# Optimization experiments

Measured on AMD Instinct MI355X. Metric: run time of the kernel, lower is better.

The kernel has to match this reference:

```python
import jax, jax.numpy as jnp
import numpy as np

EPS = 1e-6
NUM_HEADS = 8


def setup_inputs() -> dict:
    key0 = jax.random.key(0)
    ks = jax.random.split(key0, 8)
    N, B, C, HW = 900, 8, 256, 1156

    def lin(k):
        kw, kb = jax.random.split(k)
        W = jax.random.normal(kw, (C, C), jnp.float32) * 0.02
        b = jax.random.normal(kb, (C,), jnp.float32) * 0.02
        return W, b

    Wq, bq = lin(ks[0])
    Wk, bk = lin(ks[1])
    Wv, bv = lin(ks[2])
    Wo, bo = lin(ks[3])
    query = jax.random.normal(ks[4], (N, B, C), jnp.float32)
    key = jax.random.normal(ks[5], (HW, B, C), jnp.float32)
    query_pos = jax.random.normal(ks[6], (N, B, C), jnp.float32)
    key_pos = jax.random.normal(ks[7], (HW, B, C), jnp.float32)
    return dict(query=query, key=key, query_pos=query_pos, key_pos=key_pos,
                Wq=Wq, bq=bq, Wk=Wk, bk=bk, Wv=Wv, bv=bv, Wo=Wo, bo=bo)


def reference(query, key, query_pos, key_pos, Wq, bq, Wk, bk, Wv, bv, Wo, bo):
    # Faithful port of LinearCrossAttention.forward (value=None -> key,
    # identity=None -> query, batch_first=False, dropout inactive).
    # NOTE: the original permutes to (B, seq, head, head_dim) but then applies
    # cumsum(dim=2) / einsums along axis 2, i.e. over the HEAD axis; we
    # reproduce that exactly.
    N, B, C = query.shape
    HW = key.shape[0]
    H = NUM_HEADS
    D = C // H

    q = (query @ Wq.T + bq) + query_pos          # (N,B,C)
    k = (key @ Wk.T + bk) + key_pos              # (HW,B,C)
    v = key @ Wv.T + bv                          # (HW,B,C)

    q = jnp.transpose(q.reshape(N, B, H, D), (1, 0, 2, 3))    # (B,N,H,D)
    k = jnp.transpose(k.reshape(HW, B, H, D), (1, 0, 2, 3))   # (B,HW,H,D)
    v = jnp.transpose(v.reshape(HW, B, H, D), (1, 0, 2, 3))   # (B,HW,H,D)

    q = jax.nn.sigmoid(q)
    k = jax.nn.sigmoid(k)

    if HW > N:  # pad queries along the sequence axis
        q = jnp.concatenate([q, jnp.zeros((B, HW - N, H, D), q.dtype)], axis=1)

    dot = lambda a, b: jnp.sum(a * b, axis=-1)   # 'nhld,nhld->nhl'

    sink_incoming = 1.0 / dot(q + EPS, jnp.cumsum(k, axis=2) + EPS)   # (B,HW,H)
    source_outgoing = 1.0 / dot(k + EPS, jnp.cumsum(q, axis=2) + EPS)
    normal = (jnp.arange(H, dtype=q.dtype) + 1.0)[None, None, :]       # (1,1,H)
    sink_incoming = sink_incoming * normal
    source_outgoing = source_outgoing * normal

    conserved_sink = dot(q + EPS, jnp.cumsum(k * source_outgoing[..., None], axis=2) + EPS) / normal
    conserved_source = dot(k + EPS, jnp.cumsum(q * sink_incoming[..., None], axis=2) + EPS) / normal
    conserved_source = jnp.clip(conserved_source, -1.0, 1.0)

    sink_allocation = jax.nn.sigmoid(conserved_sink)
    conserved_source = jnp.exp(conserved_source)
    source_competition = conserved_source / jnp.cumsum(conserved_source, axis=-1) * normal

    # causal_dot_product with cumsum over axis 2 (head axis in this layout)
    qs = q * (sink_incoming[..., None] / normal[..., None])            # (B,HW,H,D)
    kv = jnp.cumsum(jnp.einsum('blhd,blhm->blhdm', k, v * source_competition[..., None]), axis=2)
    qkv = jnp.einsum('blhd,blhdm->blhm', qs, kv)                       # (B,HW,H,D)

    out = (qkv * sink_allocation[..., None])[:, :N]                    # (B,N,H,D)
    out = jnp.swapaxes(out, 1, 2).reshape(B, N, C)                     # matches torch transpose(1,2).reshape
    out = out @ Wo.T + bo
    out = jnp.swapaxes(out, 0, 1)                                      # (N,B,C)
    return query + out
```

## Files before the change

### kernel.cpp

```cpp
#include <hip/hip_runtime.h>
#include <math.h>

#define EPSV 1e-6f
constexpr int N_ = 900, B_ = 8, C_ = 256, H_ = 8, D_ = 32;
constexpr int M_TOT = N_ * B_;
constexpr int BM  = 32;
constexpr int NBLK = M_TOT / BM;
constexpr int BM2 = 32;
constexpr int VS  = 272;
constexpr int OFF_AQ = 65536;
constexpr int OFF_AK = 81920;
constexpr int OFF_Q  = 98304;
constexpr int OFF_K  = OFF_Q + BM * VS * 2;
constexpr int OFF_V  = OFF_K + BM * VS * 2;
constexpr int LDS1   = OFF_V + BM * VS * 2;
constexpr int LDS2   = 81920;

typedef __attribute__((ext_vector_type(8))) short short8;
typedef __attribute__((ext_vector_type(4))) float f32x4;
typedef __attribute__((ext_vector_type(4))) unsigned short us4;

__device__ __forceinline__ unsigned short f2bf(float f) {
    unsigned int u = __float_as_uint(f);
    return (unsigned short)((u + 0x7FFFu + ((u >> 16) & 1u)) >> 16);
}
__device__ __forceinline__ float bf2f(unsigned short u) {
    return __uint_as_float(((unsigned int)u) << 16);
}
__device__ __forceinline__ int swz(int row, int kElem) {
    int b = (row << 9) + (kElem << 1);
    return b ^ ((row & 7) << 4);
}
__device__ __forceinline__ float red8(float v) {
    v += __shfl_xor(v, 1); v += __shfl_xor(v, 2); v += __shfl_xor(v, 4);
    return v;
}

__global__ __launch_bounds__(256)
void pack_w(const float* __restrict__ Wq, const float* __restrict__ Wk,
            const float* __restrict__ Wv, const float* __restrict__ Wo,
            unsigned short* __restrict__ wbf)
{
    const int i = (blockIdx.x * 256 + threadIdx.x) * 8;
    const float* src = (i < 65536) ? Wq : (i < 131072) ? Wk
                     : (i < 196608) ? Wv : Wo;
    const int off = i & 65535;
    const float4 a = *reinterpret_cast<const float4*>(src + off);
    const float4 b = *reinterpret_cast<const float4*>(src + off + 4);
    short8 p;
    p[0]=(short)f2bf(a.x); p[1]=(short)f2bf(a.y);
    p[2]=(short)f2bf(a.z); p[3]=(short)f2bf(a.w);
    p[4]=(short)f2bf(b.x); p[5]=(short)f2bf(b.y);
    p[6]=(short)f2bf(b.z); p[7]=(short)f2bf(b.w);
    *reinterpret_cast<short8*>(wbf + i) = p;
}

__device__ __forceinline__ void stageW(const unsigned short* Wmat, int kkElem,
                                       char* wbufLds, int cw, int lane)
{
    #pragma unroll
    for (int n = 0; n < 8; ++n) {
        const int L  = n * 1024 + lane * 16;
        const int cl = L >> 7;
        const int kb = (L & 127) ^ ((cl & 7) << 4);
        const char* src = (const char*)Wmat + (size_t)(cw + cl) * 512
                        + kkElem * 2 + kb;
        __builtin_amdgcn_global_load_lds(
            (const __attribute__((address_space(1))) unsigned int*)src,
            (__attribute__((address_space(3))) unsigned int*)(wbufLds + n * 1024),
            16, 0, 0);
    }
}

__device__ __forceinline__ void step_mm(const unsigned char* At, const char* wb,
                                        int kkA, int lrow, int kg8,
                                        f32x4 acc[2][4])
{
    #pragma unroll
    for (int kh = 0; kh < 2; ++kh) {
        const short8 a0 = *reinterpret_cast<const short8*>(At + swz(lrow,      kkA + kh*32 + kg8));
        const short8 a1 = *reinterpret_cast<const short8*>(At + swz(16 + lrow, kkA + kh*32 + kg8));
        #pragma unroll
        for (int j = 0; j < 4; ++j) {
            const int cl = j*16 + lrow;
            const short8 bfr = *reinterpret_cast<const short8*>(
                wb + cl*128 + ((kh*64 + kg8*2) ^ ((cl & 7) << 4)));
            acc[0][j] = __builtin_amdgcn_mfma_f32_16x16x32_bf16(a0, bfr, acc[0][j], 0, 0, 0);
            acc[1][j] = __builtin_amdgcn_mfma_f32_16x16x32_bf16(a1, bfr, acc[1][j], 0, 0, 0);
        }
    }
}

__global__ __launch_bounds__(256)
void fused_qkva(const float* __restrict__ query, const float* __restrict__ key,
                const float* __restrict__ qpos,  const float* __restrict__ kpos,
                const unsigned short* __restrict__ wbf,
                const float* __restrict__ bq, const float* __restrict__ bk,
                const float* __restrict__ bv,
                unsigned short* __restrict__ abf)
{
    extern __shared__ char smem[];
    char* Wb = smem;
    unsigned char* Aq = (unsigned char*)(smem + OFF_AQ);
    unsigned char* Ak = (unsigned char*)(smem + OFF_AK);
    unsigned short* q_sb = (unsigned short*)(smem + OFF_Q);
    unsigned short* k_sb = (unsigned short*)(smem + OFF_K);
    unsigned short* v_sb = (unsigned short*)(smem + OFF_V);

    const int tid = threadIdx.x;
    const int r0  = blockIdx.x * BM;
    const int wave = tid >> 6, lane = tid & 63;
    const int cw = wave * 64;
    char* mywb = Wb + wave * 16384;

    stageW(wbf, 0, mywb, cw, lane);

    {
        const int trow = tid >> 5, k0 = (tid & 31) * 8;
        #pragma unroll
        for (int i = 0; i < 4; ++i) {
            const int row = trow + i * 8;
            const float* xr = query + (size_t)(r0 + row) * C_ + k0;
            const float4 a0 = *reinterpret_cast<const float4*>(xr);
            const float4 a1 = *reinterpret_cast<const float4*>(xr + 4);
            short8 pa;
            pa[0]=(short)f2bf(a0.x); pa[1]=(short)f2bf(a0.y);
            pa[2]=(short)f2bf(a0.z); pa[3]=(short)f2bf(a0.w);
            pa[4]=(short)f2bf(a1.x); pa[5]=(short)f2bf(a1.y);
            pa[6]=(short)f2bf(a1.z); pa[7]=(short)f2bf(a1.w);
            *reinterpret_cast<short8*>(Aq + swz(row, k0)) = pa;
            const float* kr = key + (size_t)(r0 + row) * C_ + k0;
            const float4 b0 = *reinterpret_cast<const float4*>(kr);
            const float4 b1 = *reinterpret_cast<const float4*>(kr + 4);
            short8 pb;
            pb[0]=(short)f2bf(b0.x); pb[1]=(short)f2bf(b0.y);
            pb[2]=(short)f2bf(b0.z); pb[3]=(short)f2bf(b0.w);
            pb[4]=(short)f2bf(b1.x); pb[5]=(short)f2bf(b1.y);
            pb[6]=(short)f2bf(b1.z); pb[7]=(short)f2bf(b1.w);
            *reinterpret_cast<short8*>(Ak + swz(row, k0)) = pb;
        }
    }

    const int lrow = lane & 15, kg8 = (lane >> 4) * 8;
    const int crow0 = (lane >> 4) * 4, ccol = lane & 15;

    float qp[32], kp[32], bqv[4], bkv[4], bvv[4];
    #pragma unroll
    for (int j = 0; j < 4; ++j) {
        const int ch = cw + j*16 + ccol;
        bqv[j] = bq[ch]; bkv[j] = bk[ch]; bvv[j] = bv[ch];
        #pragma unroll
        for (int rh = 0; rh < 2; ++rh)
            #pragma unroll
            for (int r_ = 0; r_ < 4; ++r_) {
                const int gr = r0 + rh*16 + crow0 + r_;
                qp[j*8+rh*4+r_] = qpos[(size_t)gr * C_ + ch];
                kp[j*8+rh*4+r_] = kpos[(size_t)gr * C_ + ch];
            }
    }

    __syncthreads();

    f32x4 qacc[2][4] = {}; f32x4 kacc[2][4] = {}; f32x4 vacc[2][4] = {};

    #pragma unroll
    for (int s = 0; s < 12; ++s) {
        if (s < 11) {
            const int nx = s + 1;
            stageW(wbf + (nx >> 2) * 65536, (nx & 3) * 64,
                   mywb + (nx & 1) * 8192, cw, lane);
            asm volatile("s_waitcnt vmcnt(8)" ::: "memory");
        } else {
            asm volatile("s_waitcnt vmcnt(0)" ::: "memory");
        }

        const char* wb = mywb + (s & 1) * 8192;
        const int kkA = (s & 3) * 64;
        if (s < 4)      step_mm(Aq, wb, kkA, lrow, kg8, qacc);
        else if (s < 8) step_mm(Ak, wb, kkA, lrow, kg8, kacc);
        else            step_mm(Ak, wb, kkA, lrow, kg8, vacc);

        if (s == 3) {
            #pragma unroll
            for (int j = 0; j < 4; ++j) {
                const int ch = cw + j*16 + ccol;
                #pragma unroll
                for (int rh = 0; rh < 2; ++rh)
                    #pragma unroll
                    for (int r_ = 0; r_ < 4; ++r_) {
                        float v = qacc[rh][j][r_] + bqv[j] + qp[j*8+rh*4+r_];
                        q_sb[(rh*16+crow0+r_)*VS + ch] = f2bf(1.f/(1.f+expf(-v)));
                    }
            }
        }
        if (s == 7) {
            #pragma unroll
            for (int j = 0; j < 4; ++j) {
                const int ch = cw + j*16 + ccol;
                #pragma unroll
                for (int rh = 0; rh < 2; ++rh)
                    #pragma unroll
                    for (int r_ = 0; r_ < 4; ++r_) {
                        float v = kacc[rh][j][r_] + bkv[j] + kp[j*8+rh*4+r_];
                        k_sb[(rh*16+crow0+r_)*VS + ch] = f2bf(1.f/(1.f+expf(-v)));
                    }
            }
        }
        if (s == 11) {
            #pragma unroll
            for (int j = 0; j < 4; ++j) {
                const int ch = cw + j*16 + ccol;
                #pragma unroll
                for (int rh = 0; rh < 2; ++rh)
                    #pragma unroll
                    for (int r_ = 0; r_ < 4; ++r_)
                        v_sb[(rh*16+crow0+r_)*VS + ch] =
                            f2bf(vacc[rh][j][r_] + bvv[j]);
            }
        }
    }

    __syncthreads();

    {
        const int loc = tid >> 3, tt = tid & 7, d0 = tt * 4;
        const int gr = r0 + loc;
        const int nn = gr >> 3, bb = gr & 7;
        const unsigned short* qr = q_sb + loc * VS + d0;
        const unsigned short* kr = k_sb + loc * VS + d0;
        const unsigned short* vr = v_sb + loc * VS + d0;
        f32x4 qh[8], kh[8], vh[8];
        #pragma unroll
        for (int h = 0; h < 8; ++h) {
            const us4 tq = *reinterpret_cast<const us4*>(qr + (h << 5));
            const us4 tk = *reinterpret_cast<const us4*>(kr + (h << 5));
            const us4 tv = *reinterpret_cast<const us4*>(vr + (h << 5));
            #pragma unroll
            for (int j = 0; j < 4; ++j) {
                qh[h][j] = bf2f(tq[j]); kh[h][j] = bf2f(tk[j]); vh[h][j] = bf2f(tv[j]);
            }
        }

        float ir1[8], so_[8];
        {
            f32x4 ck = {0,0,0,0}, cq = {0,0,0,0};
            #pragma unroll
            for (int h = 0; h < 8; ++h) {
                float p1 = 0.f, p2 = 0.f;
                #pragma unroll
                for (int j = 0; j < 4; ++j) {
                    ck[j] += kh[h][j]; cq[j] += qh[h][j];
                    p1 += (qh[h][j] + EPSV) * (ck[j] + EPSV);
                    p2 += (kh[h][j] + EPSV) * (cq[j] + EPSV);
                }
                p1 = red8(p1); p2 = red8(p2);
                ir1[h] = 1.f / p1;
                so_[h] = (float)(h+1) / p2;
            }
        }
        float salloc[8], scomp[8];
        {
            f32x4 c2 = {0,0,0,0}, c3 = {0,0,0,0};
            float css = 0.f;
            #pragma unroll
            for (int h = 0; h < 8; ++h) {
                const float sih = (float)(h+1) * ir1[h];
                float p3 = 0.f, p4 = 0.f;
                #pragma unroll
                for (int j = 0; j < 4; ++j) {
                    c2[j] += kh[h][j] * so_[h];
                    c3[j] += qh[h][j] * sih;
                    p3 += (qh[h][j] + EPSV) * (c2[j] + EPSV);
                    p4 += (kh[h][j] + EPSV) * (c3[j] + EPSV);
                }
                p3 = red8(p3); p4 = red8(p4);
                const float inv_n = 1.f / (float)(h+1);
                salloc[h] = 1.f / (1.f + expf(-p3 * inv_n));
                const float consrc = fminf(1.f, fmaxf(-1.f, p4 * inv_n));
                const float cs = expf(consrc);
                css += cs;
                scomp[h] = cs / css * (float)(h+1);
            }
        }
        #pragma unroll
        for (int h = 0; h < 8; ++h) {
            f32x4 qs4, a4 = {0,0,0,0};
            #pragma unroll
            for (int j = 0; j < 4; ++j) qs4[j] = qh[h][j] * ir1[h];
            #pragma unroll
            for (int h2 = 0; h2 <= h; ++h2) {
                float p = 0.f;
                #pragma unroll
                for (int j = 0; j < 4; ++j) p += qs4[j] * kh[h2][j];
                p = red8(p);
                const float w = p * scomp[h2];
                #pragma unroll
                for (int j = 0; j < 4; ++j) a4[j] += w * vh[h2][j];
            }
            us4 o;
            #pragma unroll
            for (int j = 0; j < 4; ++j) o[j] = f2bf(a4[j] * salloc[h]);
            *reinterpret_cast<us4*>(abf + (size_t)bb*(H_*N_*D_) + (size_t)h*(N_*D_)
                                        + (size_t)nn*D_ + d0) = o;
        }
    }
}

__global__ __launch_bounds__(256, 2)
void outproj(const unsigned short* __restrict__ abf,
             const unsigned short* __restrict__ wbf,
             const float* __restrict__ bo,
             const float* __restrict__ query,
             float* __restrict__ out)
{
    extern __shared__ char smem[];
    char* Wb = smem;
    unsigned char* As = (unsigned char*)(smem + 65536);
    const int tid = threadIdx.x;
    const int r0  = blockIdx.x * BM2;
    const int wave = tid >> 6, lane = tid & 63;
    const int cw = wave * 64;
    char* mywb = Wb + wave * 16384;
    const unsigned short* Wo = wbf + 3*65536;

    stageW(Wo, 0, mywb, cw, lane);

    {
        const int trow = tid >> 5, k0 = (tid & 31) * 8;
        #pragma unroll
        for (int i = 0; i < 4; ++i) {
            const int row = trow + i * 8;
            const int gr = r0 + row;
            const int nn = gr >> 3, bb = gr & 7;
            const short8 p = *reinterpret_cast<const short8*>(
                abf + (size_t)bb * (N_*C_) + (size_t)nn * C_ + k0);
            *reinterpret_cast<short8*>(As + swz(row, k0)) = p;
        }
    }

    const int lrow = lane & 15, kg8 = (lane >> 4) * 8;
    const int crow0 = (lane >> 4) * 4, ccol = lane & 15;

    float bov[4], qres[32];
    #pragma unroll
    for (int j = 0; j < 4; ++j) {
        const int ch = cw + j*16 + ccol;
        bov[j] = bo[ch];
        #pragma unroll
        for (int rh = 0; rh < 2; ++rh)
            #pragma unroll
            for (int r_ = 0; r_ < 4; ++r_)
                qres[j*8+rh*4+r_] =
                    query[(size_t)(r0 + rh*16 + crow0 + r_) * C_ + ch];
    }

    __syncthreads();

    f32x4 acc[2][4] = {};
    #pragma unroll
    for (int s = 0; s < 4; ++s) {
        if (s < 3) {
            stageW(Wo, (s+1)*64, mywb + ((s+1) & 1) * 8192, cw, lane);
            asm volatile("s_waitcnt vmcnt(8)" ::: "memory");
        } else {
            asm volatile("s_waitcnt vmcnt(0)" ::: "memory");
        }
        step_mm(As, mywb + (s & 1) * 8192, s*64, lrow, kg8, acc);
    }

    #pragma unroll
    for (int j = 0; j < 4; ++j) {
        const int ch = cw + j*16 + ccol;
        #pragma unroll
        for (int rh = 0; rh < 2; ++rh)
            #pragma unroll
            for (int r_ = 0; r_ < 4; ++r_) {
                const size_t g = (size_t)(r0 + rh*16 + crow0 + r_) * C_ + ch;
                out[g] = acc[rh][j][r_] + bov[j] + qres[j*8+rh*4+r_];
            }
    }
}

extern "C" void kernel_launch(void* const* d_in, const int* in_sizes, int n_in,
                              void* d_out, int out_size, void* d_ws, size_t ws_size,
                              hipStream_t stream)
{
    const float* query = (const float*)d_in[0];
    const float* key   = (const float*)d_in[1];
    const float* qpos  = (const float*)d_in[2];
    const float* kpos  = (const float*)d_in[3];
    const float* Wq = (const float*)d_in[4];  const float* bq = (const float*)d_in[5];
    const float* Wk = (const float*)d_in[6];  const float* bk = (const float*)d_in[7];
    const float* Wv = (const float*)d_in[8];  const float* bv = (const float*)d_in[9];
    const float* Wo = (const float*)d_in[10]; const float* bo = (const float*)d_in[11];

    unsigned short* wbf = (unsigned short*)d_ws;
    unsigned short* abf = wbf + 4*65536;
    float* out = (float*)d_out;

    pack_w<<<128, 256, 0, stream>>>(Wq, Wk, Wv, Wo, wbf);
    fused_qkva<<<NBLK, 256, LDS1, stream>>>(query, key, qpos, kpos, wbf,
                                            bq, bk, bv, abf);
    outproj<<<NBLK, 256, LDS2, stream>>>(abf, wbf, bo, query, out);
}
```

Baseline: 35.79 us.

## Fuse QKV projection, attention and output projection into one per-batch-chunk kernel

Merges the QKV/attention kernel and the output-projection kernel into one launch. Each block now handles a chunk of queries for one batch index, with a wrap-around overlap of extra rows, so the scrambled reshape mapping the output projection needs can be resolved in LDS. This removes the bf16 intermediate round trip through global memory and one kernel launch. In exchange, each block computes QKV for 32 rows but only uses 20 of them for output, which wastes matrix work and idles part of the output-projection MFMA tile.

```diff
diff --git a/kernel.cpp b/kernel.cpp
--- a/kernel.cpp
+++ b/kernel.cpp
@@ -3,18 +3,17 @@
 
 #define EPSV 1e-6f
 constexpr int N_ = 900, B_ = 8, C_ = 256, H_ = 8, D_ = 32;
-constexpr int M_TOT = N_ * B_;
-constexpr int BM  = 32;
-constexpr int NBLK = M_TOT / BM;
-constexpr int BM2 = 32;
+constexpr int L_  = 20;
+constexpr int S_  = 24;
+constexpr int NCH = N_ / L_;
 constexpr int VS  = 272;
+constexpr int AOS = 264;
 constexpr int OFF_AQ = 65536;
 constexpr int OFF_AK = 81920;
 constexpr int OFF_Q  = 98304;
-constexpr int OFF_K  = OFF_Q + BM * VS * 2;
-constexpr int OFF_V  = OFF_K + BM * VS * 2;
-constexpr int LDS1   = OFF_V + BM * VS * 2;
-constexpr int LDS2   = 81920;
+constexpr int OFF_K  = OFF_Q + 32 * VS * 2;
+constexpr int OFF_V  = OFF_K + 32 * VS * 2;
+constexpr int LDS1   = OFF_V + 32 * VS * 2;
 
 typedef __attribute__((ext_vector_type(8))) short short8;
 typedef __attribute__((ext_vector_type(4))) float f32x4;
@@ -92,12 +91,12 @@
 }
 
 __global__ __launch_bounds__(256)
-void fused_qkva(const float* __restrict__ query, const float* __restrict__ key,
-                const float* __restrict__ qpos,  const float* __restrict__ kpos,
-                const unsigned short* __restrict__ wbf,
-                const float* __restrict__ bq, const float* __restrict__ bk,
-                const float* __restrict__ bv,
-                unsigned short* __restrict__ abf)
+void lca_all(const float* __restrict__ query, const float* __restrict__ key,
+             const float* __restrict__ qpos,  const float* __restrict__ kpos,
+             const unsigned short* __restrict__ wbf,
+             const float* __restrict__ bq, const float* __restrict__ bk,
+             const float* __restrict__ bv, const float* __restrict__ bo,
+             float* __restrict__ out)
 {
     extern __shared__ char smem[];
     char* Wb = smem;
@@ -106,9 +105,12 @@
     unsigned short* q_sb = (unsigned short*)(smem + OFF_Q);
     unsigned short* k_sb = (unsigned short*)(smem + OFF_K);
     unsigned short* v_sb = (unsigned short*)(smem + OFF_V);
+    unsigned short* aO   = (unsigned short*)(smem + OFF_AK);
 
     const int tid = threadIdx.x;
-    const int r0  = blockIdx.x * BM;
+    const int ic  = blockIdx.x;
+    const int b   = blockIdx.y;
+    const int s   = ic * L_;
     const int wave = tid >> 6, lane = tid & 63;
     const int cw = wave * 64;
     char* mywb = Wb + wave * 16384;
@@ -120,18 +122,18 @@
         #pragma unroll
         for (int i = 0; i < 4; ++i) {
             const int row = trow + i * 8;
-            const float* xr = query + (size_t)(r0 + row) * C_ + k0;
-            const float4 a0 = *reinterpret_cast<const float4*>(xr);
-            const float4 a1 = *reinterpret_cast<const float4*>(xr + 4);
+            int n2 = s + row; if (n2 >= N_) n2 -= N_;
+            const size_t base = (size_t)(n2 * B_ + b) * C_ + k0;
+            const float4 a0 = *reinterpret_cast<const float4*>(query + base);
+            const float4 a1 = *reinterpret_cast<const float4*>(query + base + 4);
             short8 pa;
             pa[0]=(short)f2bf(a0.x); pa[1]=(short)f2bf(a0.y);
             pa[2]=(short)f2bf(a0.z); pa[3]=(short)f2bf(a0.w);
             pa[4]=(short)f2bf(a1.x); pa[5]=(short)f2bf(a1.y);
             pa[6]=(short)f2bf(a1.z); pa[7]=(short)f2bf(a1.w);
             *reinterpret_cast<short8*>(Aq + swz(row, k0)) = pa;
-            const float* kr = key + (size_t)(r0 + row) * C_ + k0;
-            const float4 b0 = *reinterpret_cast<const float4*>(kr);
-            const float4 b1 = *reinterpret_cast<const float4*>(kr + 4);
+            const float4 b0 = *reinterpret_cast<const float4*>(key + base);
+            const float4 b1 = *reinterpret_cast<const float4*>(key + base + 4);
             short8 pb;
             pb[0]=(short)f2bf(b0.x); pb[1]=(short)f2bf(b0.y);
             pb[2]=(short)f2bf(b0.z); pb[3]=(short)f2bf(b0.w);
@@ -144,18 +146,20 @@
     const int lrow = lane & 15, kg8 = (lane >> 4) * 8;
     const int crow0 = (lane >> 4) * 4, ccol = lane & 15;
 
-    float qp[32], kp[32], bqv[4], bkv[4], bvv[4];
+    float qp[32], kp[32], bqv[4], bkv[4], bvv[4], bov[4];
     #pragma unroll
     for (int j = 0; j < 4; ++j) {
         const int ch = cw + j*16 + ccol;
-        bqv[j] = bq[ch]; bkv[j] = bk[ch]; bvv[j] = bv[ch];
+        bqv[j] = bq[ch]; bkv[j] = bk[ch]; bvv[j] = bv[ch]; bov[j] = bo[ch];
         #pragma unroll
         for (int rh = 0; rh < 2; ++rh)
             #pragma unroll
             for (int r_ = 0; r_ < 4; ++r_) {
-                const int gr = r0 + rh*16 + crow0 + r_;
-                qp[j*8+rh*4+r_] = qpos[(size_t)gr * C_ + ch];
-                kp[j*8+rh*4+r_] = kpos[(size_t)gr * C_ + ch];
+                const int row = rh*16 + crow0 + r_;
+                int n2 = s + row; if (n2 >= N_) n2 -= N_;
+                const size_t g = (size_t)(n2 * B_ + b) * C_ + ch;
+                qp[j*8+rh*4+r_] = qpos[g];
+                kp[j*8+rh*4+r_] = kpos[g];
             }
     }
 
@@ -164,9 +168,9 @@
     f32x4 qacc[2][4] = {}; f32x4 kacc[2][4] = {}; f32x4 vacc[2][4] = {};
 
     #pragma unroll
-    for (int s = 0; s < 12; ++s) {
-        if (s < 11) {
-            const int nx = s + 1;
+    for (int st = 0; st < 12; ++st) {
+        if (st < 11) {
+            const int nx = st + 1;
             stageW(wbf + (nx >> 2) * 65536, (nx & 3) * 64,
                    mywb + (nx & 1) * 8192, cw, lane);
             asm volatile("s_waitcnt vmcnt(8)" ::: "memory");
@@ -174,13 +178,13 @@
             asm volatile("s_waitcnt vmcnt(0)" ::: "memory");
         }
 
-        const char* wb = mywb + (s & 1) * 8192;
-        const int kkA = (s & 3) * 64;
-        if (s < 4)      step_mm(Aq, wb, kkA, lrow, kg8, qacc);
-        else if (s < 8) step_mm(Ak, wb, kkA, lrow, kg8, kacc);
-        else            step_mm(Ak, wb, kkA, lrow, kg8, vacc);
-
-        if (s == 3) {
+        const char* wb = mywb + (st & 1) * 8192;
+        const int kkA = (st & 3) * 64;
+        if (st < 4)      step_mm(Aq, wb, kkA, lrow, kg8, qacc);
+        else if (st < 8) step_mm(Ak, wb, kkA, lrow, kg8, kacc);
+        else             step_mm(Ak, wb, kkA, lrow, kg8, vacc);
+
+        if (st == 3) {
             #pragma unroll
             for (int j = 0; j < 4; ++j) {
                 const int ch = cw + j*16 + ccol;
@@ -193,7 +197,7 @@
                     }
             }
         }
-        if (s == 7) {
+        if (st == 7) {
             #pragma unroll
             for (int j = 0; j < 4; ++j) {
                 const int ch = cw + j*16 + ccol;
@@ -206,7 +210,7 @@
                     }
             }
         }
-        if (s == 11) {
+        if (st == 11) {
             #pragma unroll
             for (int j = 0; j < 4; ++j) {
                 const int ch = cw + j*16 + ccol;
@@ -222,162 +226,141 @@
 
     __syncthreads();
 
+    stageW(wbf + 3*65536, 0, mywb, cw, lane);
+
     {
         const int loc = tid >> 3, tt = tid & 7, d0 = tt * 4;
-        const int gr = r0 + loc;
-        const int nn = gr >> 3, bb = gr & 7;
-        const unsigned short* qr = q_sb + loc * VS + d0;
-        const unsigned short* kr = k_sb + loc * VS + d0;
-        const unsigned short* vr = v_sb + loc * VS + d0;
-        f32x4 qh[8], kh[8], vh[8];
-        #pragma unroll
-        for (int h = 0; h < 8; ++h) {
-            const us4 tq = *reinterpret_cast<const us4*>(qr + (h << 5));
-            const us4 tk = *reinterpret_cast<const us4*>(kr + (h << 5));
-            const us4 tv = *reinterpret_cast<const us4*>(vr + (h << 5));
-            #pragma unroll
-            for (int j = 0; j < 4; ++j) {
-                qh[h][j] = bf2f(tq[j]); kh[h][j] = bf2f(tk[j]); vh[h][j] = bf2f(tv[j]);
-            }
-        }
-
-        float ir1[8], so_[8];
-        {
-            f32x4 ck = {0,0,0,0}, cq = {0,0,0,0};
+        if (loc < S_) {
+            const unsigned short* qr = q_sb + loc * VS + d0;
+            const unsigned short* kr = k_sb + loc * VS + d0;
+            const unsigned short* vr = v_sb + loc * VS + d0;
+            f32x4 qh[8], kh[8], vh[8];
             #pragma unroll
             for (int h = 0; h < 8; ++h) {
-                float p1 = 0.f, p2 = 0.f;
+                const us4 tq = *reinterpret_cast<const us4*>(qr + (h << 5));
+                const us4 tk = *reinterpret_cast<const us4*>(kr + (h << 5));
+                const us4 tv = *reinterpret_cast<const us4*>(vr + (h << 5));
                 #pragma unroll
                 for (int j = 0; j < 4; ++j) {
-                    ck[j] += kh[h][j]; cq[j] += qh[h][j];
-                    p1 += (qh[h][j] + EPSV) * (ck[j] + EPSV);
-                    p2 += (kh[h][j] + EPSV) * (cq[j] + EPSV);
-                }
-                p1 = red8(p1); p2 = red8(p2);
-                ir1[h] = 1.f / p1;
-                so_[h] = (float)(h+1) / p2;
-            }
-        }
-        float salloc[8], scomp[8];
-        {
-            f32x4 c2 = {0,0,0,0}, c3 = {0,0,0,0};
-            float css = 0.f;
+                    qh[h][j] = bf2f(tq[j]); kh[h][j] = bf2f(tk[j]); vh[h][j] = bf2f(tv[j]);
+                }
+            }
+
+            float ir1[8], so_[8];
+            {
+                f32x4 ck = {0,0,0,0}, cq = {0,0,0,0};
+                #pragma unroll
+                for (int h = 0; h < 8; ++h) {
+                    float p1 = 0.f, p2 = 0.f;
+                    #pragma unroll
+                    for (int j = 0; j < 4; ++j) {
+                        ck[j] += kh[h][j]; cq[j] += qh[h][j];
+                        p1 += (qh[h][j] + EPSV) * (ck[j] + EPSV);
+                        p2 += (kh[h][j] + EPSV) * (cq[j] + EPSV);
+                    }
+                    p1 = red8(p1); p2 = red8(p2);
+                    ir1[h] = 1.f / p1;
+                    so_[h] = (float)(h+1) / p2;
+                }
+            }
+            float salloc[8], scomp[8];
+            {
+                f32x4 c2 = {0,0,0,0}, c3 = {0,0,0,0};
+                float css = 0.f;
+                #pragma unroll
+                for (int h = 0; h < 8; ++h) {
+                    const float sih = (float)(h+1) * ir1[h];
+                    float p3 = 0.f, p4 = 0.f;
+                    #pragma unroll
+                    for (int j = 0; j < 4; ++j) {
+                        c2[j] += kh[h][j] * so_[h];
+                        c3[j] += qh[h][j] * sih;
+                        p3 += (qh[h][j] + EPSV) * (c2[j] + EPSV);
+                        p4 += (kh[h][j] + EPSV) * (c3[j] + EPSV);
+                    }
+                    p3 = red8(p3); p4 = red8(p4);
+                    const float inv_n = 1.f / (float)(h+1);
+                    salloc[h] = 1.f / (1.f + expf(-p3 * inv_n));
+                    const float consrc = fminf(1.f, fmaxf(-1.f, p4 * inv_n));
+                    const float cs = expf(consrc);
+                    css += cs;
+                    scomp[h] = cs / css * (float)(h+1);
+                }
+            }
             #pragma unroll
             for (int h = 0; h < 8; ++h) {
-                const float sih = (float)(h+1) * ir1[h];
-                float p3 = 0.f, p4 = 0.f;
-                #pragma unroll
-                for (int j = 0; j < 4; ++j) {
-                    c2[j] += kh[h][j] * so_[h];
-                    c3[j] += qh[h][j] * sih;
-                    p3 += (qh[h][j] + EPSV) * (c2[j] + EPSV);
-                    p4 += (kh[h][j] + EPSV) * (c3[j] + EPSV);
-                }
-                p3 = red8(p3); p4 = red8(p4);
-                const float inv_n = 1.f / (float)(h+1);
-                salloc[h] = 1.f / (1.f + expf(-p3 * inv_n));
-                const float consrc = fminf(1.f, fmaxf(-1.f, p4 * inv_n));
-                const float cs = expf(consrc);
-                css += cs;
-                scomp[h] = cs / css * (float)(h+1);
-            }
-        }
-        #pragma unroll
-        for (int h = 0; h < 8; ++h) {
-            f32x4 qs4, a4 = {0,0,0,0};
-            #pragma unroll
-            for (int j = 0; j < 4; ++j) qs4[j] = qh[h][j] * ir1[h];
-            #pragma unroll
-            for (int h2 = 0; h2 <= h; ++h2) {
-                float p = 0.f;
-                #pragma unroll
-                for (int j = 0; j < 4; ++j) p += qs4[j] * kh[h2][j];
-                p = red8(p);
-                const float w = p * scomp[h2];
-                #pragma unroll
-                for (int j = 0; j < 4; ++j) a4[j] += w * vh[h2][j];
-            }
-            us4 o;
-            #pragma unroll
-            for (int j = 0; j < 4; ++j) o[j] = f2bf(a4[j] * salloc[h]);
-            *reinterpret_cast<us4*>(abf + (size_t)bb*(H_*N_*D_) + (size_t)h*(N_*D_)
-                                        + (size_t)nn*D_ + d0) = o;
-        }
-    }
-}
-
-__global__ __launch_bounds__(256, 2)
-void outproj(const unsigned short* __restrict__ abf,
-             const unsigned short* __restrict__ wbf,
-             const float* __restrict__ bo,
-             const float* __restrict__ query,
-             float* __restrict__ out)
-{
-    extern __shared__ char smem[];
-    char* Wb = smem;
-    unsigned char* As = (unsigned char*)(smem + 65536);
-    const int tid = threadIdx.x;
-    const int r0  = blockIdx.x * BM2;
-    const int wave = tid >> 6, lane = tid & 63;
-    const int cw = wave * 64;
-    char* mywb = Wb + wave * 16384;
-    const unsigned short* Wo = wbf + 3*65536;
-
-    stageW(Wo, 0, mywb, cw, lane);
+                f32x4 qs4, a4 = {0,0,0,0};
+                #pragma unroll
+                for (int j = 0; j < 4; ++j) qs4[j] = qh[h][j] * ir1[h];
+                #pragma unroll
+                for (int h2 = 0; h2 <= h; ++h2) {
+                    float p = 0.f;
+                    #pragma unroll
+                    for (int j = 0; j < 4; ++j) p += qs4[j] * kh[h2][j];
+                    p = red8(p);
+                    const float w = p * scomp[h2];
+                    #pragma unroll
+                    for (int j = 0; j < 4; ++j) a4[j] += w * vh[h2][j];
+                }
+                us4 o;
+                #pragma unroll
+                for (int j = 0; j < 4; ++j) o[j] = f2bf(a4[j] * salloc[h]);
+                *reinterpret_cast<us4*>(aO + loc*AOS + (h << 5) + d0) = o;
+            }
+        }
+    }
+    __syncthreads();
 
     {
-        const int trow = tid >> 5, k0 = (tid & 31) * 8;
-        #pragma unroll
-        for (int i = 0; i < 4; ++i) {
-            const int row = trow + i * 8;
-            const int gr = r0 + row;
-            const int nn = gr >> 3, bb = gr & 7;
-            const short8 p = *reinterpret_cast<const short8*>(
-                abf + (size_t)bb * (N_*C_) + (size_t)nn * C_ + k0);
-            *reinterpret_cast<short8*>(As + swz(row, k0)) = p;
-        }
-    }
-
-    const int lrow = lane & 15, kg8 = (lane >> 4) * 8;
-    const int crow0 = (lane >> 4) * 4, ccol = lane & 15;
-
-    float bov[4], qres[32];
-    #pragma unroll
-    for (int j = 0; j < 4; ++j) {
-        const int ch = cw + j*16 + ccol;
-        bov[j] = bo[ch];
-        #pragma unroll
-        for (int rh = 0; rh < 2; ++rh)
-            #pragma unroll
-            for (int r_ = 0; r_ < 4; ++r_)
-                qres[j*8+rh*4+r_] =
-                    query[(size_t)(r0 + rh*16 + crow0 + r_) * C_ + ch];
-    }
-
+        const int row_a = tid >> 3, seg = tid & 7;
+        if (row_a < L_) {
+            const int jA = row_a >> 2, kA = row_a & 3;
+            const int n  = (113 * (5*ic + jA)) % 225 + 225 * kA;
+            const int h  = (8 * n + seg) / 900;
+            const unsigned short* srcp = aO + (4*jA + seg) * AOS + (h << 5);
+            #pragma unroll
+            for (int m = 0; m < 4; ++m) {
+                const short8 v = *reinterpret_cast<const short8*>(srcp + m*8);
+                *reinterpret_cast<short8*>(Aq + swz(row_a, seg*32 + m*8)) = v;
+            }
+        } else {
+            const short8 z = {0,0,0,0,0,0,0,0};
+            #pragma unroll
+            for (int m = 0; m < 4; ++m)
+                *reinterpret_cast<short8*>(Aq + swz(row_a, seg*32 + m*8)) = z;
+        }
+    }
     __syncthreads();
 
-    f32x4 acc[2][4] = {};
-    #pragma unroll
-    for (int s = 0; s < 4; ++s) {
-        if (s < 3) {
-            stageW(Wo, (s+1)*64, mywb + ((s+1) & 1) * 8192, cw, lane);
-            asm volatile("s_waitcnt vmcnt(8)" ::: "memory");
-        } else {
-            asm volatile("s_waitcnt vmcnt(0)" ::: "memory");
-        }
-        step_mm(As, mywb + (s & 1) * 8192, s*64, lrow, kg8, acc);
-    }
-
-    #pragma unroll
-    for (int j = 0; j < 4; ++j) {
-        const int ch = cw + j*16 + ccol;
-        #pragma unroll
-        for (int rh = 0; rh < 2; ++rh)
-            #pragma unroll
-            for (int r_ = 0; r_ < 4; ++r_) {
-                const size_t g = (size_t)(r0 + rh*16 + crow0 + r_) * C_ + ch;
-                out[g] = acc[rh][j][r_] + bov[j] + qres[j*8+rh*4+r_];
-            }
+    {
+        f32x4 oacc[2][4] = {};
+        #pragma unroll
+        for (int sp = 0; sp < 4; ++sp) {
+            if (sp < 3) {
+                stageW(wbf + 3*65536, (sp+1)*64, mywb + ((sp+1) & 1) * 8192, cw, lane);
+                asm volatile("s_waitcnt vmcnt(8)" ::: "memory");
+            } else {
+                asm volatile("s_waitcnt vmcnt(0)" ::: "memory");
+            }
+            step_mm(Aq, mywb + (sp & 1) * 8192, sp*64, lrow, kg8, oacc);
+        }
+
+        #pragma unroll
+        for (int j = 0; j < 4; ++j) {
+            const int ch = cw + j*16 + ccol;
+            #pragma unroll
+            for (int rh = 0; rh < 2; ++rh)
+                #pragma unroll
+                for (int r_ = 0; r_ < 4; ++r_) {
+                    const int row_a = rh*16 + crow0 + r_;
+                    if (row_a < L_) {
+                        const int jA = row_a >> 2, kA = row_a & 3;
+                        const int n  = (113 * (5*ic + jA)) % 225 + 225 * kA;
+                        const size_t g = (size_t)(n * B_ + b) * C_ + ch;
+                        out[g] = oacc[rh][j][r_] + bov[j] + query[g];
+                    }
+                }
+        }
     }
 }
 
@@ -395,11 +378,9 @@
     const float* Wo = (const float*)d_in[10]; const float* bo = (const float*)d_in[11];
 
     unsigned short* wbf = (unsigned short*)d_ws;
-    unsigned short* abf = wbf + 4*65536;
     float* out = (float*)d_out;
 
     pack_w<<<128, 256, 0, stream>>>(Wq, Wk, Wv, Wo, wbf);
-    fused_qkva<<<NBLK, 256, LDS1, stream>>>(query, key, qpos, kpos, wbf,
-                                            bq, bk, bv, abf);
-    outproj<<<NBLK, 256, LDS2, stream>>>(abf, wbf, bo, query, out);
-}
+    lca_all<<<dim3(NCH, B_), 256, LDS1, stream>>>(
+        query, key, qpos, kpos, wbf, bq, bk, bv, bo, out);
+}
```

Measured after the change: 62.77 us. +75.4%, slower.

## Double threads per block to 512, splitting output columns across eight waves

Applied to the files above, without the earlier changes.

Both GEMM kernels now launch 512 threads (eight waves), each wave owning 32 output columns instead of 64. Weight staging, accumulators and register arrays are halved per wave. The attention epilogue spreads each row over 16 lanes with 2 elements each, using 16-lane shuffle reductions. The aim is more parallelism per block and less register pressure per thread, at the cost of more shuffle reductions and per-wave A-fragment reloads.

```diff
diff --git a/kernel.cpp b/kernel.cpp
--- a/kernel.cpp
+++ b/kernel.cpp
@@ -6,7 +6,6 @@
 constexpr int M_TOT = N_ * B_;
 constexpr int BM  = 32;
 constexpr int NBLK = M_TOT / BM;
-constexpr int BM2 = 32;
 constexpr int VS  = 272;
 constexpr int OFF_AQ = 65536;
 constexpr int OFF_AK = 81920;
@@ -18,7 +17,8 @@
 
 typedef __attribute__((ext_vector_type(8))) short short8;
 typedef __attribute__((ext_vector_type(4))) float f32x4;
-typedef __attribute__((ext_vector_type(4))) unsigned short us4;
+typedef __attribute__((ext_vector_type(2))) float f32x2;
+typedef __attribute__((ext_vector_type(2))) unsigned short us2;
 
 __device__ __forceinline__ unsigned short f2bf(float f) {
     unsigned int u = __float_as_uint(f);
@@ -31,8 +31,9 @@
     int b = (row << 9) + (kElem << 1);
     return b ^ ((row & 7) << 4);
 }
-__device__ __forceinline__ float red8(float v) {
-    v += __shfl_xor(v, 1); v += __shfl_xor(v, 2); v += __shfl_xor(v, 4);
+__device__ __forceinline__ float red16(float v) {
+    v += __shfl_xor(v, 1); v += __shfl_xor(v, 2);
+    v += __shfl_xor(v, 4); v += __shfl_xor(v, 8);
     return v;
 }
 
@@ -55,11 +56,11 @@
     *reinterpret_cast<short8*>(wbf + i) = p;
 }
 
-__device__ __forceinline__ void stageW(const unsigned short* Wmat, int kkElem,
-                                       char* wbufLds, int cw, int lane)
-{
-    #pragma unroll
-    for (int n = 0; n < 8; ++n) {
+__device__ __forceinline__ void stageW32(const unsigned short* Wmat, int kkElem,
+                                         char* wbufLds, int cw, int lane)
+{
+    #pragma unroll
+    for (int n = 0; n < 4; ++n) {
         const int L  = n * 1024 + lane * 16;
         const int cl = L >> 7;
         const int kb = (L & 127) ^ ((cl & 7) << 4);
@@ -72,16 +73,16 @@
     }
 }
 
-__device__ __forceinline__ void step_mm(const unsigned char* At, const char* wb,
-                                        int kkA, int lrow, int kg8,
-                                        f32x4 acc[2][4])
+__device__ __forceinline__ void step_mm32(const unsigned char* At, const char* wb,
+                                          int kkA, int lrow, int kg8,
+                                          f32x4 acc[2][2])
 {
     #pragma unroll
     for (int kh = 0; kh < 2; ++kh) {
         const short8 a0 = *reinterpret_cast<const short8*>(At + swz(lrow,      kkA + kh*32 + kg8));
         const short8 a1 = *reinterpret_cast<const short8*>(At + swz(16 + lrow, kkA + kh*32 + kg8));
         #pragma unroll
-        for (int j = 0; j < 4; ++j) {
+        for (int j = 0; j < 2; ++j) {
             const int cl = j*16 + lrow;
             const short8 bfr = *reinterpret_cast<const short8*>(
                 wb + cl*128 + ((kh*64 + kg8*2) ^ ((cl & 7) << 4)));
@@ -91,7 +92,7 @@
     }
 }
 
-__global__ __launch_bounds__(256)
+__global__ __launch_bounds__(512)
 void fused_qkva(const float* __restrict__ query, const float* __restrict__ key,
                 const float* __restrict__ qpos,  const float* __restrict__ kpos,
                 const unsigned short* __restrict__ wbf,
@@ -110,16 +111,16 @@
     const int tid = threadIdx.x;
     const int r0  = blockIdx.x * BM;
     const int wave = tid >> 6, lane = tid & 63;
-    const int cw = wave * 64;
-    char* mywb = Wb + wave * 16384;
-
-    stageW(wbf, 0, mywb, cw, lane);
+    const int cw = wave * 32;
+    char* mywb = Wb + wave * 8192;
+
+    stageW32(wbf, 0, mywb, cw, lane);
 
     {
         const int trow = tid >> 5, k0 = (tid & 31) * 8;
         #pragma unroll
-        for (int i = 0; i < 4; ++i) {
-            const int row = trow + i * 8;
+        for (int i = 0; i < 2; ++i) {
+            const int row = trow + i * 16;
             const float* xr = query + (size_t)(r0 + row) * C_ + k0;
             const float4 a0 = *reinterpret_cast<const float4*>(xr);
             const float4 a1 = *reinterpret_cast<const float4*>(xr + 4);
@@ -144,9 +145,9 @@
     const int lrow = lane & 15, kg8 = (lane >> 4) * 8;
     const int crow0 = (lane >> 4) * 4, ccol = lane & 15;
 
-    float qp[32], kp[32], bqv[4], bkv[4], bvv[4];
-    #pragma unroll
-    for (int j = 0; j < 4; ++j) {
+    float qp[16], kp[16], bqv[2], bkv[2], bvv[2];
+    #pragma unroll
+    for (int j = 0; j < 2; ++j) {
         const int ch = cw + j*16 + ccol;
         bqv[j] = bq[ch]; bkv[j] = bk[ch]; bvv[j] = bv[ch];
         #pragma unroll
@@ -161,28 +162,28 @@
 
     __syncthreads();
 
-    f32x4 qacc[2][4] = {}; f32x4 kacc[2][4] = {}; f32x4 vacc[2][4] = {};
-
-    #pragma unroll
-    for (int s = 0; s < 12; ++s) {
-        if (s < 11) {
-            const int nx = s + 1;
-            stageW(wbf + (nx >> 2) * 65536, (nx & 3) * 64,
-                   mywb + (nx & 1) * 8192, cw, lane);
-            asm volatile("s_waitcnt vmcnt(8)" ::: "memory");
+    f32x4 qacc[2][2] = {}; f32x4 kacc[2][2] = {}; f32x4 vacc[2][2] = {};
+
+    #pragma unroll
+    for (int st = 0; st < 12; ++st) {
+        if (st < 11) {
+            const int nx = st + 1;
+            stageW32(wbf + (nx >> 2) * 65536, (nx & 3) * 64,
+                     mywb + (nx & 1) * 4096, cw, lane);
+            asm volatile("s_waitcnt vmcnt(4)" ::: "memory");
         } else {
             asm volatile("s_waitcnt vmcnt(0)" ::: "memory");
         }
 
-        const char* wb = mywb + (s & 1) * 8192;
-        const int kkA = (s & 3) * 64;
-        if (s < 4)      step_mm(Aq, wb, kkA, lrow, kg8, qacc);
-        else if (s < 8) step_mm(Ak, wb, kkA, lrow, kg8, kacc);
-        else            step_mm(Ak, wb, kkA, lrow, kg8, vacc);
-
-        if (s == 3) {
-            #pragma unroll
-            for (int j = 0; j < 4; ++j) {
+        const char* wb = mywb + (st & 1) * 4096;
+        const int kkA = (st & 3) * 64;
+        if (st < 4)      step_mm32(Aq, wb, kkA, lrow, kg8, qacc);
+        else if (st < 8) step_mm32(Ak, wb, kkA, lrow, kg8, kacc);
+        else             step_mm32(Ak, wb, kkA, lrow, kg8, vacc);
+
+        if (st == 3) {
+            #pragma unroll
+            for (int j = 0; j < 2; ++j) {
                 const int ch = cw + j*16 + ccol;
                 #pragma unroll
                 for (int rh = 0; rh < 2; ++rh)
@@ -193,9 +194,9 @@
                     }
             }
         }
-        if (s == 7) {
-            #pragma unroll
-            for (int j = 0; j < 4; ++j) {
+        if (st == 7) {
+            #pragma unroll
+            for (int j = 0; j < 2; ++j) {
                 const int ch = cw + j*16 + ccol;
                 #pragma unroll
                 for (int rh = 0; rh < 2; ++rh)
@@ -206,9 +207,9 @@
                     }
             }
         }
-        if (s == 11) {
-            #pragma unroll
-            for (int j = 0; j < 4; ++j) {
+        if (st == 11) {
+            #pragma unroll
+            for (int j = 0; j < 2; ++j) {
                 const int ch = cw + j*16 + ccol;
                 #pragma unroll
                 for (int rh = 0; rh < 2; ++rh)
@@ -223,57 +224,56 @@
     __syncthreads();
 
     {
-        const int loc = tid >> 3, tt = tid & 7, d0 = tt * 4;
+        const int loc = tid >> 4, tt = tid & 15, d0 = tt * 2;
         const int gr = r0 + loc;
         const int nn = gr >> 3, bb = gr & 7;
         const unsigned short* qr = q_sb + loc * VS + d0;
         const unsigned short* kr = k_sb + loc * VS + d0;
         const unsigned short* vr = v_sb + loc * VS + d0;
-        f32x4 qh[8], kh[8], vh[8];
+        f32x2 qh[8], kh[8], vh[8];
         #pragma unroll
         for (int h = 0; h < 8; ++h) {
-            const us4 tq = *reinterpret_cast<const us4*>(qr + (h << 5));
-            const us4 tk = *reinterpret_cast<const us4*>(kr + (h << 5));
-            const us4 tv = *reinterpret_cast<const us4*>(vr + (h << 5));
-            #pragma unroll
-            for (int j = 0; j < 4; ++j) {
-                qh[h][j] = bf2f(tq[j]); kh[h][j] = bf2f(tk[j]); vh[h][j] = bf2f(tv[j]);
-            }
+            const us2 tq = *reinterpret_cast<const us2*>(qr + (h << 5));
+            const us2 tk = *reinterpret_cast<const us2*>(kr + (h << 5));
+            const us2 tv = *reinterpret_cast<const us2*>(vr + (h << 5));
+            qh[h][0] = bf2f(tq[0]); qh[h][1] = bf2f(tq[1]);
+            kh[h][0] = bf2f(tk[0]); kh[h][1] = bf2f(tk[1]);
+            vh[h][0] = bf2f(tv[0]); vh[h][1] = bf2f(tv[1]);
         }
 
         float ir1[8], so_[8];
         {
-            f32x4 ck = {0,0,0,0}, cq = {0,0,0,0};
+            f32x2 ck = {0,0}, cq = {0,0};
             #pragma unroll
             for (int h = 0; h < 8; ++h) {
                 float p1 = 0.f, p2 = 0.f;
                 #pragma unroll
-                for (int j = 0; j < 4; ++j) {
+                for (int j = 0; j < 2; ++j) {
                     ck[j] += kh[h][j]; cq[j] += qh[h][j];
                     p1 += (qh[h][j] + EPSV) * (ck[j] + EPSV);
                     p2 += (kh[h][j] + EPSV) * (cq[j] + EPSV);
                 }
-                p1 = red8(p1); p2 = red8(p2);
+                p1 = red16(p1); p2 = red16(p2);
                 ir1[h] = 1.f / p1;
                 so_[h] = (float)(h+1) / p2;
             }
         }
         float salloc[8], scomp[8];
         {
-            f32x4 c2 = {0,0,0,0}, c3 = {0,0,0,0};
+            f32x2 c2 = {0,0}, c3 = {0,0};
             float css = 0.f;
             #pragma unroll
             for (int h = 0; h < 8; ++h) {
                 const float sih = (float)(h+1) * ir1[h];
                 float p3 = 0.f, p4 = 0.f;
                 #pragma unroll
-                for (int j = 0; j < 4; ++j) {
+                for (int j = 0; j < 2; ++j) {
                     c2[j] += kh[h][j] * so_[h];
                     c3[j] += qh[h][j] * sih;
                     p3 += (qh[h][j] + EPSV) * (c2[j] + EPSV);
                     p4 += (kh[h][j] + EPSV) * (c3[j] + EPSV);
                 }
-                p3 = red8(p3); p4 = red8(p4);
+                p3 = red16(p3); p4 = red16(p4);
                 const float inv_n = 1.f / (float)(h+1);
                 salloc[h] = 1.f / (1.f + expf(-p3 * inv_n));
                 const float consrc = fminf(1.f, fmaxf(-1.f, p4 * inv_n));
@@ -284,29 +284,29 @@
         }
         #pragma unroll
         for (int h = 0; h < 8; ++h) {
-            f32x4 qs4, a4 = {0,0,0,0};
-            #pragma unroll
-            for (int j = 0; j < 4; ++j) qs4[j] = qh[h][j] * ir1[h];
+            f32x2 qs2, a2 = {0,0};
+            #pragma unroll
+            for (int j = 0; j < 2; ++j) qs2[j] = qh[h][j] * ir1[h];
             #pragma unroll
             for (int h2 = 0; h2 <= h; ++h2) {
                 float p = 0.f;
                 #pragma unroll
-                for (int j = 0; j < 4; ++j) p += qs4[j] * kh[h2][j];
-                p = red8(p);
+                for (int j = 0; j < 2; ++j) p += qs2[j] * kh[h2][j];
+                p = red16(p);
                 const float w = p * scomp[h2];
                 #pragma unroll
-                for (int j = 0; j < 4; ++j) a4[j] += w * vh[h2][j];
-            }
-            us4 o;
-            #pragma unroll
-            for (int j = 0; j < 4; ++j) o[j] = f2bf(a4[j] * salloc[h]);
-            *reinterpret_cast<us4*>(abf + (size_t)bb*(H_*N_*D_) + (size_t)h*(N_*D_)
+                for (int j = 0; j < 2; ++j) a2[j] += w * vh[h2][j];
+            }
+            us2 o;
+            o[0] = f2bf(a2[0] * salloc[h]);
+            o[1] = f2bf(a2[1] * salloc[h]);
+            *reinterpret_cast<us2*>(abf + (size_t)bb*(H_*N_*D_) + (size_t)h*(N_*D_)
                                         + (size_t)nn*D_ + d0) = o;
         }
     }
 }
 
-__global__ __launch_bounds__(256, 2)
+__global__ __launch_bounds__(512)
 void outproj(const unsigned short* __restrict__ abf,
              const unsigned short* __restrict__ wbf,
              const float* __restrict__ bo,
@@ -317,19 +317,19 @@
     char* Wb = smem;
     unsigned char* As = (unsigned char*)(smem + 65536);
     const int tid = threadIdx.x;
-    const int r0  = blockIdx.x * BM2;
+    const int r0  = blockIdx.x * BM;
     const int wave = tid >> 6, lane = tid & 63;
-    const int cw = wave * 64;
-    char* mywb = Wb + wave * 16384;
+    const int cw = wave * 32;
+    char* mywb = Wb + wave * 8192;
     const unsigned short* Wo = wbf + 3*65536;
 
-    stageW(Wo, 0, mywb, cw, lane);
+    stageW32(Wo, 0, mywb, cw, lane);
 
     {
         const int trow = tid >> 5, k0 = (tid & 31) * 8;
         #pragma unroll
-        for (int i = 0; i < 4; ++i) {
-            const int row = trow + i * 8;
+        for (int i = 0; i < 2; ++i) {
+            const int row = trow + i * 16;
             const int gr = r0 + row;
             const int nn = gr >> 3, bb = gr & 7;
             const short8 p = *reinterpret_cast<const short8*>(
@@ -341,9 +341,9 @@
     const int lrow = lane & 15, kg8 = (lane >> 4) * 8;
     const int crow0 = (lane >> 4) * 4, ccol = lane & 15;
 
-    float bov[4], qres[32];
-    #pragma unroll
-    for (int j = 0; j < 4; ++j) {
+    float bov[2], qres[16];
+    #pragma unroll
+    for (int j = 0; j < 2; ++j) {
         const int ch = cw + j*16 + ccol;
         bov[j] = bo[ch];
         #pragma unroll
@@ -356,20 +356,20 @@
 
     __syncthreads();
 
-    f32x4 acc[2][4] = {};
-    #pragma unroll
-    for (int s = 0; s < 4; ++s) {
-        if (s < 3) {
-            stageW(Wo, (s+1)*64, mywb + ((s+1) & 1) * 8192, cw, lane);
-            asm volatile("s_waitcnt vmcnt(8)" ::: "memory");
+    f32x4 acc[2][2] = {};
+    #pragma unroll
+    for (int sp = 0; sp < 4; ++sp) {
+        if (sp < 3) {
+            stageW32(Wo, (sp+1)*64, mywb + ((sp+1) & 1) * 4096, cw, lane);
+            asm volatile("s_waitcnt vmcnt(4)" ::: "memory");
         } else {
             asm volatile("s_waitcnt vmcnt(0)" ::: "memory");
         }
-        step_mm(As, mywb + (s & 1) * 8192, s*64, lrow, kg8, acc);
-    }
-
-    #pragma unroll
-    for (int j = 0; j < 4; ++j) {
+        step_mm32(As, mywb + (sp & 1) * 4096, sp*64, lrow, kg8, acc);
+    }
+
+    #pragma unroll
+    for (int j = 0; j < 2; ++j) {
         const int ch = cw + j*16 + ccol;
         #pragma unroll
         for (int rh = 0; rh < 2; ++rh)
@@ -399,7 +399,7 @@
     float* out = (float*)d_out;
 
     pack_w<<<128, 256, 0, stream>>>(Wq, Wk, Wv, Wo, wbf);
-    fused_qkva<<<NBLK, 256, LDS1, stream>>>(query, key, qpos, kpos, wbf,
+    fused_qkva<<<NBLK, 512, LDS1, stream>>>(query, key, qpos, kpos, wbf,
                                             bq, bk, bv, abf);
-    outproj<<<NBLK, 256, LDS2, stream>>>(abf, wbf, bo, query, out);
-}
+    outproj<<<NBLK, 512, LDS2, stream>>>(abf, wbf, bo, query, out);
+}
```

After: 34.26 us. -4.3%, faster.
